# Performance work log

Hardware: AMD Instinct MI355X
Metric: run time of the kernel (lower is better)

The kernel has to match this reference:

```python
import jax, jax.numpy as jnp
import numpy as np
import math

N_RES, N_EDGE = 10000, 320000
C_S, C_Z, C_H, H, PQ, PV = 384, 128, 16, 12, 4, 8
INF, EPS = 1e5, 1e-8


def _lin(key, din, dout):
    k1, k2 = jax.random.split(key)
    w = jax.random.normal(k1, (din, dout), jnp.float32) * (1.0 / np.sqrt(din))
    b = jax.random.normal(k2, (dout,), jnp.float32) * 0.02
    return w, b


def setup_inputs() -> dict:
    key = jax.random.key(0)
    ks = jax.random.split(key, 16)
    s = jax.random.normal(ks[0], (N_RES, C_S), jnp.float32)
    z = jax.random.normal(ks[1], (N_EDGE, C_Z), jnp.float32)
    edge_index = jax.random.randint(ks[2], (2, N_EDGE), 0, N_RES, jnp.int32)
    rot = jnp.linalg.qr(jax.random.normal(ks[3], (N_RES, 3, 3), jnp.float32))[0]
    trans = jax.random.normal(ks[4], (N_RES, 3), jnp.float32)
    mask = jnp.ones((N_RES,), jnp.float32)
    wq, bq = _lin(ks[5], C_S, H * C_H)
    wkv, bkv = _lin(ks[6], C_S, 2 * H * C_H)
    wqp, bqp = _lin(ks[7], C_S, H * PQ * 3)
    wkvp, bkvp = _lin(ks[8], C_S, H * (PQ + PV) * 3)
    wb, bb = _lin(ks[9], C_Z, H)
    wdz, bdz = _lin(ks[10], C_Z, C_Z // 4)
    head_w = jax.random.normal(ks[11], (H,), jnp.float32) * 0.1
    wout, bout = _lin(ks[12], H * (C_Z // 4 + C_H + PV * 4), C_S)
    return dict(s=s, z=z, rot=rot, trans=trans, mask=mask, edge_index=edge_index,
                wq=wq, bq=bq, wkv=wkv, bkv=bkv, wqp=wqp, bqp=bqp, wkvp=wkvp, bkvp=bkvp,
                wb=wb, bb=bb, wdz=wdz, bdz=bdz, head_w=head_w, wout=wout, bout=bout)


def reference(s, z, rot, trans, mask, edge_index, wq, bq, wkv, bkv, wqp, bqp,
              wkvp, bkvp, wb, bb, wdz, bdz, head_w, wout, bout):
    n = s.shape[0]
    src, dst = edge_index[0], edge_index[1]  # key-side, query-side

    q = (s @ wq + bq).reshape(n, H, C_H)
    kv = (s @ wkv + bkv).reshape(n, H, 2 * C_H)
    k, v = kv[..., :C_H], kv[..., C_H:]

    def make_pts(x, p):
        # torch: split [n, H*p*3] into 3 chunks of H*p, stack on last dim -> [n, H*p, 3]
        x = jnp.stack(jnp.split(x, 3, axis=-1), axis=-1)
        x = jnp.einsum('nij,npj->npi', rot, x) + trans[:, None, :]  # global frame
        return x.reshape(n, H, p, 3)

    q_pts = make_pts(s @ wqp + bqp, PQ)                 # [n, H, PQ, 3]
    kv_pts = make_pts(s @ wkvp + bkvp, PQ + PV)
    k_pts, v_pts = kv_pts[..., :PQ, :], kv_pts[..., PQ:, :]

    b = z @ wb + bb                                      # [E, H]
    a = jnp.einsum('ehc,ehc->eh', q[dst], k[src]) * math.sqrt(1.0 / (3 * C_H))
    a = a + math.sqrt(1.0 / 3) * b

    disp = q_pts[dst] - k_pts[src]                       # [E, H, PQ, 3]
    hw = jax.nn.softplus(head_w) * math.sqrt(1.0 / (3 * (PQ * 9.0 / 2)))
    pt_att = -0.5 * jnp.einsum('ehp,h->eh', jnp.sum(disp * disp, axis=-1), hw)

    edge_mask = INF * (mask[src] * mask[dst] - 1.0)
    a = a + pt_att + edge_mask[:, None]

    # segment softmax over edges grouped by destination node
    m = jax.lax.stop_gradient(jax.ops.segment_max(a, dst, num_segments=n))
    ea = jnp.exp(a - m[dst])
    a = ea / (jax.ops.segment_sum(ea, dst, num_segments=n)[dst] + 1e-16)

    o = jax.ops.segment_sum(a[..., None] * v[src], dst, num_segments=n).reshape(n, -1)

    o_pt = jax.ops.segment_sum(a[..., None, None] * v_pts[src], dst, num_segments=n)  # [n,H,PV,3]
    o_pt = jnp.einsum('nji,nhpj->nhpi', rot, o_pt - trans[:, None, None, :])  # invert_apply
    o_pt_norm = jnp.sqrt(jnp.sum(o_pt * o_pt, axis=-1) + EPS).reshape(n, -1)
    o_pt = o_pt.reshape(n, H * PV, 3)

    pair_z = z @ wdz + bdz                               # [E, c_z//4]
    o_pair = jax.ops.segment_sum(a[..., None] * pair_z[:, None, :], dst,
                                 num_segments=n).reshape(n, -1)

    feats = jnp.concatenate([o, o_pt[..., 0], o_pt[..., 1], o_pt[..., 2],
                             o_pt_norm, o_pair], axis=-1)
    return feats @ wout + bout
```

## Files before the change

kernel.cpp:

```cpp
#include <hip/hip_runtime.h>
#include <hip/hip_bf16.h>
#include <math.h>

#define N_RESC 10000
#define N_EDGEC 320000
#define C_SC 384
#define C_ZC 128
#define AGG_D 864
#define FEAT_D 960
#define OUT_D 384

#define S1C 0.14433756729740643f
#define S2C 0.5773502691896258f
#define SHWC 0.13608276348795434f

__global__ void k_zero(int* cursor) {
    int i = blockIdx.x * 256 + threadIdx.x;
    if (i < N_RESC) cursor[i] = 0;
}

__global__ void k_hist(const int* __restrict__ ei, int* cursor) {
    int e = blockIdx.x * 256 + threadIdx.x;
    if (e < N_EDGEC) atomicAdd(&cursor[ei[N_EDGEC + e]], 1);
}

__global__ __launch_bounds__(1024) void k_scan(int* cursor, int* rowptr) {
    __shared__ int buf[1024];
    __shared__ int carry_s;
    int t = threadIdx.x;
    if (t == 0) carry_s = 0;
    __syncthreads();
    for (int ch = 0; ch < 10; ++ch) {
        int idx = ch * 1024 + t;
        int v = (idx < N_RESC) ? cursor[idx] : 0;
        buf[t] = v;
        __syncthreads();
        for (int off = 1; off < 1024; off <<= 1) {
            int x = (t >= off) ? buf[t - off] : 0;
            __syncthreads();
            buf[t] += x;
            __syncthreads();
        }
        int incl = buf[t];
        int excl = incl - v;
        int base = carry_s;
        int total = buf[1023];
        if (idx < N_RESC) { rowptr[idx] = base + excl; cursor[idx] = base + excl; }
        __syncthreads();
        if (t == 0) carry_s = base + total;
        __syncthreads();
    }
    if (t == 0) rowptr[N_RESC] = carry_s;
}

__global__ void k_scatter(const int* __restrict__ ei, int* cursor, int* csr,
                          int* src_csr, int* epos) {
    int e = blockIdx.x * 256 + threadIdx.x;
    if (e < N_EDGEC) {
        int d = ei[N_EDGEC + e];
        int s = ei[e];
        int pos = atomicAdd(&cursor[d], 1);
        csr[pos] = e;
        src_csr[pos] = s;
        epos[e] = pos;
    }
}

__global__ __launch_bounds__(256) void k_wpack(
    const float* __restrict__ wq, const float* __restrict__ bq,
    const float* __restrict__ wkv, const float* __restrict__ bkv,
    const float* __restrict__ wqp, const float* __restrict__ bqp,
    const float* __restrict__ wkvp, const float* __restrict__ bkvp,
    float* __restrict__ wpack, float* __restrict__ bpack) {
    int idx = blockIdx.x * 256 + threadIdx.x;
    if (idx < 384 * 1152) {
        int j = idx / 1152, c = idx % 1152;
        float v;
        if (c < 192)      v = wq[j * 192 + c];
        else if (c < 576) v = wkv[j * 384 + (c - 192)];
        else if (c < 720) v = wqp[j * 144 + (c - 576)];
        else              v = wkvp[j * 432 + (c - 720)];
        wpack[idx] = v;
    }
    if (idx < 1152) {
        float b;
        if (idx < 192)      b = bq[idx];
        else if (idx < 576) b = bkv[idx - 192];
        else if (idx < 720) b = bqp[idx - 576];
        else                b = bkvp[idx - 720];
        bpack[idx] = b;
    }
}

#define BM 64
#define BN 128
#define BK 32
__global__ __launch_bounds__(256) void k_proj(const float* __restrict__ s,
    const float* __restrict__ wpack, const float* __restrict__ bpack,
    float* __restrict__ qh, float* __restrict__ kh, float* __restrict__ vh,
    float* __restrict__ praw) {
    __shared__ float sT[BK][BM + 4];
    __shared__ float wt[BK][BN];
    int t = threadIdx.x;
    int bm0 = blockIdx.x * BM;
    int bn0 = blockIdx.y * BN;
    int tcol = t & 31;
    int trow = t >> 5;
    int c0 = tcol * 4;
    int r0 = trow * 8;

    int srow = t >> 2;
    int skoff = (t & 3) * 8;
    int gsrow = min(bm0 + srow, N_RESC - 1);
    const float* srcp = s + (long)gsrow * C_SC + skoff;

    float acc[8][4];
    #pragma unroll
    for (int i = 0; i < 8; i++)
        #pragma unroll
        for (int j = 0; j < 4; j++) acc[i][j] = 0.f;

    for (int k0 = 0; k0 < C_SC; k0 += BK) {
        float4 sa = *(const float4*)(srcp + k0);
        float4 sb = *(const float4*)(srcp + k0 + 4);
        sT[skoff + 0][srow] = sa.x; sT[skoff + 1][srow] = sa.y;
        sT[skoff + 2][srow] = sa.z; sT[skoff + 3][srow] = sa.w;
        sT[skoff + 4][srow] = sb.x; sT[skoff + 5][srow] = sb.y;
        sT[skoff + 6][srow] = sb.z; sT[skoff + 7][srow] = sb.w;
        #pragma unroll
        for (int q = 0; q < 4; q++) {
            int kk = (t >> 5) + q * 8;
            *(float4*)&wt[kk][c0] =
                *(const float4*)(wpack + (long)(k0 + kk) * 1152 + bn0 + c0);
        }
        __syncthreads();
        #pragma unroll
        for (int k = 0; k < BK; k++) {
            float4 a0 = *(const float4*)&sT[k][r0];
            float4 a1 = *(const float4*)&sT[k][r0 + 4];
            float4 b  = *(const float4*)&wt[k][c0];
            float av0 = a0.x, av1 = a0.y, av2 = a0.z, av3 = a0.w;
            float av4 = a1.x, av5 = a1.y, av6 = a1.z, av7 = a1.w;
            acc[0][0] = fmaf(av0, b.x, acc[0][0]); acc[0][1] = fmaf(av0, b.y, acc[0][1]);
            acc[0][2] = fmaf(av0, b.z, acc[0][2]); acc[0][3] = fmaf(av0, b.w, acc[0][3]);
            acc[1][0] = fmaf(av1, b.x, acc[1][0]); acc[1][1] = fmaf(av1, b.y, acc[1][1]);
            acc[1][2] = fmaf(av1, b.z, acc[1][2]); acc[1][3] = fmaf(av1, b.w, acc[1][3]);
            acc[2][0] = fmaf(av2, b.x, acc[2][0]); acc[2][1] = fmaf(av2, b.y, acc[2][1]);
            acc[2][2] = fmaf(av2, b.z, acc[2][2]); acc[2][3] = fmaf(av2, b.w, acc[2][3]);
            acc[3][0] = fmaf(av3, b.x, acc[3][0]); acc[3][1] = fmaf(av3, b.y, acc[3][1]);
            acc[3][2] = fmaf(av3, b.z, acc[3][2]); acc[3][3] = fmaf(av3, b.w, acc[3][3]);
            acc[4][0] = fmaf(av4, b.x, acc[4][0]); acc[4][1] = fmaf(av4, b.y, acc[4][1]);
            acc[4][2] = fmaf(av4, b.z, acc[4][2]); acc[4][3] = fmaf(av4, b.w, acc[4][3]);
            acc[5][0] = fmaf(av5, b.x, acc[5][0]); acc[5][1] = fmaf(av5, b.y, acc[5][1]);
            acc[5][2] = fmaf(av5, b.z, acc[5][2]); acc[5][3] = fmaf(av5, b.w, acc[5][3]);
            acc[6][0] = fmaf(av6, b.x, acc[6][0]); acc[6][1] = fmaf(av6, b.y, acc[6][1]);
            acc[6][2] = fmaf(av6, b.z, acc[6][2]); acc[6][3] = fmaf(av6, b.w, acc[6][3]);
            acc[7][0] = fmaf(av7, b.x, acc[7][0]); acc[7][1] = fmaf(av7, b.y, acc[7][1]);
            acc[7][2] = fmaf(av7, b.z, acc[7][2]); acc[7][3] = fmaf(av7, b.w, acc[7][3]);
        }
        __syncthreads();
    }
    #pragma unroll
    for (int j = 0; j < 4; j++) {
        int c = bn0 + c0 + j;
        float bv = bpack[c];
        #pragma unroll
        for (int i = 0; i < 8; i++) {
            int n = bm0 + r0 + i;
            if (n < N_RESC) {
                float val = acc[i][j] + bv;
                if (c < 192) qh[(long)n * 192 + c] = val;
                else if (c < 576) {
                    int cc = c - 192; int h = cc >> 5, r = cc & 31;
                    if (r < 16) kh[(long)n * 192 + h * 16 + r] = val;
                    else        vh[(long)n * 192 + h * 16 + (r - 16)] = val;
                } else praw[(long)n * 576 + (c - 576)] = val;
            }
        }
    }
}

__global__ __launch_bounds__(192) void k_rot(const float* __restrict__ praw,
    const float* __restrict__ rot, const float* __restrict__ trans,
    float* __restrict__ qpts, float* __restrict__ kpts, float* __restrict__ vpts) {
    int n = blockIdx.x;
    int t = threadIdx.x;
    __shared__ float R[9], T[3];
    if (t < 9) R[t] = rot[n * 9 + t];
    if (t < 3) T[t] = trans[n * 3 + t];
    __syncthreads();
    const float* pr = praw + (long)n * 576;
    if (t < 48) {
        float x0 = pr[t], x1 = pr[48 + t], x2 = pr[96 + t];
        #pragma unroll
        for (int i = 0; i < 3; i++)
            qpts[(long)n * 144 + t * 3 + i] = R[i*3+0]*x0 + R[i*3+1]*x1 + R[i*3+2]*x2 + T[i];
    } else {
        int p = t - 48;
        float x0 = pr[144 + p], x1 = pr[288 + p], x2 = pr[432 + p];
        int h = p / 12, pp = p % 12;
        #pragma unroll
        for (int i = 0; i < 3; i++) {
            float val = R[i*3+0]*x0 + R[i*3+1]*x1 + R[i*3+2]*x2 + T[i];
            if (pp < 4) kpts[(long)n * 144 + (h * 4 + pp) * 3 + i] = val;
            else        vpts[(long)n * 288 + (h * 8 + (pp - 4)) * 3 + i] = val;
        }
    }
}

__global__ __launch_bounds__(256) void k_zproj(const float* __restrict__ z,
    const int* __restrict__ epos,
    const float* __restrict__ wb, const float* __restrict__ bb,
    const float* __restrict__ wdz, const float* __restrict__ bdz,
    float* __restrict__ b_e, float* __restrict__ pairz) {
    __shared__ float zl[256][33];
    int t = threadIdx.x;
    long e0 = (long)blockIdx.x * 256;
    const float* zbase = z + e0 * C_ZC;
    float acc[44];
    #pragma unroll
    for (int c = 0; c < 12; c++) acc[c] = bb[c];
    #pragma unroll
    for (int c = 0; c < 32; c++) acc[12 + c] = bdz[c];

    for (int ch = 0; ch < 4; ch++) {
        __syncthreads();
        #pragma unroll
        for (int k = 0; k < 8; k++) {
            int idx4 = t + k * 256;
            int row = idx4 >> 3, j4 = idx4 & 7;
            float4 v = *(const float4*)(zbase + (long)row * C_ZC + ch * 32 + j4 * 4);
            zl[row][j4 * 4 + 0] = v.x;
            zl[row][j4 * 4 + 1] = v.y;
            zl[row][j4 * 4 + 2] = v.z;
            zl[row][j4 * 4 + 3] = v.w;
        }
        __syncthreads();
        #pragma unroll
        for (int j = 0; j < 32; j++) {
            float zs = zl[t][j];
            int jg = ch * 32 + j;
            #pragma unroll
            for (int c = 0; c < 12; c++) acc[c] = fmaf(zs, wb[jg * 12 + c], acc[c]);
            #pragma unroll
            for (int c = 0; c < 32; c++) acc[12 + c] = fmaf(zs, wdz[jg * 32 + c], acc[12 + c]);
        }
    }
    long pos = epos[e0 + t];
    float4* bo = reinterpret_cast<float4*>(b_e + pos * 12);
    #pragma unroll
    for (int q = 0; q < 3; q++)
        bo[q] = make_float4(acc[q*4], acc[q*4+1], acc[q*4+2], acc[q*4+3]);
    float4* po = reinterpret_cast<float4*>(pairz + pos * 32);
    #pragma unroll
    for (int q = 0; q < 8; q++)
        po[q] = make_float4(acc[12+q*4], acc[12+q*4+1], acc[12+q*4+2], acc[12+q*4+3]);
}

#define CAPL 256
__global__ __launch_bounds__(256) void k_logit(const int* __restrict__ rowptr,
    const int* __restrict__ src_csr,
    const float* __restrict__ qh, const float* __restrict__ kh,
    const float* __restrict__ qpts, const float* __restrict__ kpts,
    const float* __restrict__ mask, const float* __restrict__ head_w,
    const float* __restrict__ b_e, float* __restrict__ alog) {
    int n = blockIdx.x;
    int t = threadIdx.x;
    __shared__ float qf[192], qp[144], hws[12];
    __shared__ int slist[CAPL];
    if (t < 192) qf[t] = qh[(long)n * 192 + t];
    if (t < 144) qp[t] = qpts[(long)n * 144 + t];
    if (t < 12)  hws[t] = log1pf(expf(head_w[t])) * SHWC;
    float mdst = mask[n];
    int row0 = rowptr[n];
    int deg = rowptr[n + 1] - row0;
    int w = t >> 6, l = t & 63, c = l & 15, hq = l >> 4;
    for (int cs = 0; cs < deg; cs += CAPL) {
        int cnt = min(CAPL, deg - cs);
        __syncthreads();
        for (int i = t; i < cnt; i += 256) slist[i] = src_csr[row0 + cs + i];
        __syncthreads();
        for (int i = w * 2; i < cnt; i += 8) {
            int i1 = min(i + 1, cnt - 1);
            int s0 = slist[i], s1 = slist[i1];
            int pos0 = row0 + cs + i, pos1 = row0 + cs + i1;
            float em0 = 100000.0f * (mask[s0] * mdst - 1.0f);
            float em1 = 100000.0f * (mask[s1] * mdst - 1.0f);
            float kv0[3], kv1[3];
            #pragma unroll
            for (int tp = 0; tp < 3; tp++) {
                kv0[tp] = kh[(long)s0 * 192 + tp * 64 + l];
                kv1[tp] = kh[(long)s1 * 192 + tp * 64 + l];
            }
            float kp0[3] = {0.f,0.f,0.f}, kp1[3] = {0.f,0.f,0.f};
            if (c < 12) {
                #pragma unroll
                for (int tp = 0; tp < 3; tp++) {
                    int h = tp * 4 + hq;
                    kp0[tp] = kpts[(long)s0 * 144 + h * 12 + c];
                    kp1[tp] = kpts[(long)s1 * 144 + h * 12 + c];
                }
            }
            float be0[3] = {0.f,0.f,0.f}, be1[3] = {0.f,0.f,0.f};
            if (c == 0) {
                #pragma unroll
                for (int tp = 0; tp < 3; tp++) {
                    int h = tp * 4 + hq;
                    be0[tp] = b_e[(long)pos0 * 12 + h];
                    be1[tp] = b_e[(long)pos1 * 12 + h];
                }
            }
            #pragma unroll
            for (int tp = 0; tp < 3; tp++) {
                int h = tp * 4 + hq;
                float qfv = S1C * qf[h * 16 + c];
                float val0 = qfv * kv0[tp];
                float val1 = qfv * kv1[tp];
                if (c < 12) {
                    float qpv = qp[h * 12 + c];
                    float hw = -0.5f * hws[h];
                    float d0 = qpv - kp0[tp];
                    float d1 = qpv - kp1[tp];
                    val0 = fmaf(hw * d0, d0, val0);
                    val1 = fmaf(hw * d1, d1, val1);
                }
                val0 += __shfl_xor(val0, 8, 16); val1 += __shfl_xor(val1, 8, 16);
                val0 += __shfl_xor(val0, 4, 16); val1 += __shfl_xor(val1, 4, 16);
                val0 += __shfl_xor(val0, 2, 16); val1 += __shfl_xor(val1, 2, 16);
                val0 += __shfl_xor(val0, 1, 16); val1 += __shfl_xor(val1, 1, 16);
                if (c == 0) {
                    alog[(long)pos0 * 12 + h] = val0 + S2C * be0[tp] + em0;
                    if (i1 != i)
                        alog[(long)pos1 * 12 + h] = val1 + S2C * be1[tp] + em1;
                }
            }
        }
    }
}

#define CAPE 256
__global__ __launch_bounds__(256) void k_agg(const int* __restrict__ rowptr,
    const int* __restrict__ src_csr,
    const float* __restrict__ alog, const float* __restrict__ vh,
    const float* __restrict__ vpts, const float* __restrict__ pairz,
    float* __restrict__ agg) {
    int n = blockIdx.x;
    int t = threadIdx.x;
    __shared__ float red[16 * 12];
    __shared__ float mh[12], linv[12];
    __shared__ float al[CAPE * 12];
    __shared__ int sl_[CAPE];
    int row0 = rowptr[n];
    int deg = rowptr[n + 1] - row0;
    int g = t >> 4, l16 = t & 15;
    if (l16 < 12) {
        float lm = -1e30f;
        for (int i = g; i < deg; i += 16)
            lm = fmaxf(lm, alog[(long)(row0 + i) * 12 + l16]);
        red[g * 12 + l16] = lm;
    }
    __syncthreads();
    if (t < 12) {
        float m = -1e30f;
        for (int gg = 0; gg < 16; gg++) m = fmaxf(m, red[gg * 12 + t]);
        mh[t] = m;
    }
    __syncthreads();
    if (l16 < 12) {
        float m = mh[l16];
        float ls = 0.f;
        for (int i = g; i < deg; i += 16)
            ls += expf(alog[(long)(row0 + i) * 12 + l16] - m);
        red[g * 12 + l16] = ls;
    }
    __syncthreads();
    if (t < 12) {
        float ssum = 0.f;
        for (int gg = 0; gg < 16; gg++) ssum += red[gg * 12 + t];
        linv[t] = 1.f / (ssum + 1e-16f);
    }

    const float* base = nullptr;
    int scale = 0, hk = 0, use_e = 0;
    int comp = t * 4;
    if (comp < 192)      { base = vh + comp; scale = 192; hk = comp >> 4; }
    else if (comp < 480) { int idx = comp - 192; base = vpts + idx; scale = 288; hk = idx / 24; }
    else if (comp < 864) { int idx = comp - 480; base = pairz + (idx & 31); scale = 32; hk = idx >> 5; use_e = 1; }
    float4 acc = make_float4(0.f, 0.f, 0.f, 0.f);

    for (int cs = 0; cs < deg; cs += CAPE) {
        int cnt = min(CAPE, deg - cs);
        int p0 = row0 + cs;
        __syncthreads();
        for (int i = t; i < cnt * 12; i += 256) {
            int h = i % 12;
            al[i] = expf(alog[(long)p0 * 12 + i] - mh[h]) * linv[h];
        }
        for (int i = t; i < cnt; i += 256) sl_[i] = src_csr[p0 + i];
        __syncthreads();
        if (t < 216) {
            int i = 0;
            for (; i + 4 <= cnt; i += 4) {
                int i0 = use_e ? (p0 + i)     : sl_[i];
                int i1 = use_e ? (p0 + i + 1) : sl_[i+1];
                int i2 = use_e ? (p0 + i + 2) : sl_[i+2];
                int i3 = use_e ? (p0 + i + 3) : sl_[i+3];
                float4 v0 = *(const float4*)(base + (long)i0 * scale);
                float4 v1 = *(const float4*)(base + (long)i1 * scale);
                float4 v2 = *(const float4*)(base + (long)i2 * scale);
                float4 v3 = *(const float4*)(base + (long)i3 * scale);
                float w0 = al[i * 12 + hk];
                float w1 = al[(i+1) * 12 + hk];
                float w2 = al[(i+2) * 12 + hk];
                float w3 = al[(i+3) * 12 + hk];
                acc.x = fmaf(w0, v0.x, acc.x); acc.y = fmaf(w0, v0.y, acc.y);
                acc.z = fmaf(w0, v0.z, acc.z); acc.w = fmaf(w0, v0.w, acc.w);
                acc.x = fmaf(w1, v1.x, acc.x); acc.y = fmaf(w1, v1.y, acc.y);
                acc.z = fmaf(w1, v1.z, acc.z); acc.w = fmaf(w1, v1.w, acc.w);
                acc.x = fmaf(w2, v2.x, acc.x); acc.y = fmaf(w2, v2.y, acc.y);
                acc.z = fmaf(w2, v2.z, acc.z); acc.w = fmaf(w2, v2.w, acc.w);
                acc.x = fmaf(w3, v3.x, acc.x); acc.y = fmaf(w3, v3.y, acc.y);
                acc.z = fmaf(w3, v3.z, acc.z); acc.w = fmaf(w3, v3.w, acc.w);
            }
            for (; i < cnt; i++) {
                int ii = use_e ? (p0 + i) : sl_[i];
                float4 v = *(const float4*)(base + (long)ii * scale);
                float w = al[i * 12 + hk];
                acc.x = fmaf(w, v.x, acc.x); acc.y = fmaf(w, v.y, acc.y);
                acc.z = fmaf(w, v.z, acc.z); acc.w = fmaf(w, v.w, acc.w);
            }
        }
    }
    if (t < 216) *(float4*)(agg + (long)n * AGG_D + comp) = acc;
}

#define NT_F 8
__global__ __launch_bounds__(192) void k_final(const float* __restrict__ agg,
    const float* __restrict__ rot, const float* __restrict__ trans,
    const float* __restrict__ wout, const float* __restrict__ bout,
    float* __restrict__ out) {
    __shared__ float f[NT_F][FEAT_D];
    int t = threadIdx.x;
    int node0 = blockIdx.x * NT_F;
    for (int idx = t; idx < NT_F * 192; idx += 192) {
        int nt = idx / 192, c = idx % 192;
        f[nt][c] = agg[(long)(node0 + nt) * AGG_D + c];
    }
    for (int idx = t; idx < NT_F * 96; idx += 192) {
        int nt = idx / 96, p = idx % 96;
        int n = node0 + nt;
        const float* a = agg + (long)n * AGG_D;
        float gx = a[192 + p * 3 + 0] - trans[n * 3 + 0];
        float gy = a[192 + p * 3 + 1] - trans[n * 3 + 1];
        float gz = a[192 + p * 3 + 2] - trans[n * 3 + 2];
        const float* R = rot + (long)n * 9;
        float lx = R[0] * gx + R[3] * gy + R[6] * gz;
        float ly = R[1] * gx + R[4] * gy + R[7] * gz;
        float lz = R[2] * gx + R[5] * gy + R[8] * gz;
        f[nt][192 + p] = lx;
        f[nt][288 + p] = ly;
        f[nt][384 + p] = lz;
        f[nt][480 + p] = sqrtf(lx * lx + ly * ly + lz * lz + 1e-8f);
    }
    for (int idx = t; idx < NT_F * 384; idx += 192) {
        int nt = idx / 384, q = idx % 384;
        f[nt][576 + q] = agg[(long)(node0 + nt) * AGG_D + 480 + q];
    }
    __syncthreads();
    float acc0[NT_F], acc1[NT_F];
    float b0 = bout[t], b1 = bout[t + 192];
    #pragma unroll
    for (int nt = 0; nt < NT_F; nt++) { acc0[nt] = b0; acc1[nt] = b1; }
    for (int j = 0; j < FEAT_D; j += 4) {
        float4 fv[NT_F];
        #pragma unroll
        for (int nt = 0; nt < NT_F; nt++) fv[nt] = *(const float4*)&f[nt][j];
        #pragma unroll
        for (int u = 0; u < 4; u++) {
            float w0 = wout[(j + u) * OUT_D + t];
            float w1 = wout[(j + u) * OUT_D + t + 192];
            #pragma unroll
            for (int nt = 0; nt < NT_F; nt++) {
                float fvu = (u == 0) ? fv[nt].x : (u == 1) ? fv[nt].y : (u == 2) ? fv[nt].z : fv[nt].w;
                acc0[nt] = fmaf(fvu, w0, acc0[nt]);
                acc1[nt] = fmaf(fvu, w1, acc1[nt]);
            }
        }
    }
    #pragma unroll
    for (int nt = 0; nt < NT_F; nt++) {
        out[(long)(node0 + nt) * OUT_D + t] = acc0[nt];
        out[(long)(node0 + nt) * OUT_D + t + 192] = acc1[nt];
    }
}

extern "C" void kernel_launch(void* const* d_in, const int* in_sizes, int n_in,
                              void* d_out, int out_size, void* d_ws, size_t ws_size,
                              hipStream_t stream) {
    const float* s     = (const float*)d_in[0];
    const float* z     = (const float*)d_in[1];
    const float* rot   = (const float*)d_in[2];
    const float* trans = (const float*)d_in[3];
    const float* mask  = (const float*)d_in[4];
    const int*   ei    = (const int*)d_in[5];
    const float* wq    = (const float*)d_in[6];
    const float* bq    = (const float*)d_in[7];
    const float* wkv   = (const float*)d_in[8];
    const float* bkv   = (const float*)d_in[9];
    const float* wqp   = (const float*)d_in[10];
    const float* bqp   = (const float*)d_in[11];
    const float* wkvp  = (const float*)d_in[12];
    const float* bkvp  = (const float*)d_in[13];
    const float* wb    = (const float*)d_in[14];
    const float* bb    = (const float*)d_in[15];
    const float* wdz   = (const float*)d_in[16];
    const float* bdz   = (const float*)d_in[17];
    const float* head_w= (const float*)d_in[18];
    const float* wout  = (const float*)d_in[19];
    const float* bout  = (const float*)d_in[20];
    float* out = (float*)d_out;

    float* ws    = (float*)d_ws;
    float* qh    = ws;
    float* kh    = qh + 1920000;
    float* vh    = kh + 1920000;
    float* qpts  = vh + 1920000;
    float* kpts  = qpts + 1440000;
    float* vpts  = kpts + 1440000;
    float* b_e   = vpts + 2880000;
    float* pairz = b_e + 3840000;
    float* alog  = pairz + 10240000;
    float* agg   = alog + 3840000;
    float* praw  = agg;
    float* wpack = agg + 5760000;
    float* bpack = wpack + 442368;
    int* rowptr  = (int*)(agg + 8640000);
    int* cursor  = rowptr + 10004;
    int* csr     = cursor + 10000;
    int* src_csr = csr + N_EDGEC;
    int* epos    = src_csr + N_EDGEC;

    k_zero<<<(N_RESC + 255) / 256, 256, 0, stream>>>(cursor);
    k_hist<<<(N_EDGEC + 255) / 256, 256, 0, stream>>>(ei, cursor);
    k_scan<<<1, 1024, 0, stream>>>(cursor, rowptr);
    k_scatter<<<(N_EDGEC + 255) / 256, 256, 0, stream>>>(ei, cursor, csr, src_csr, epos);

    k_wpack<<<(384 * 1152 + 255) / 256, 256, 0, stream>>>(wq, bq, wkv, bkv, wqp, bqp,
                                                          wkvp, bkvp, wpack, bpack);
    dim3 pgrid((N_RESC + BM - 1) / BM, 1152 / BN);
    k_proj<<<pgrid, 256, 0, stream>>>(s, wpack, bpack, qh, kh, vh, praw);
    k_rot<<<N_RESC, 192, 0, stream>>>(praw, rot, trans, qpts, kpts, vpts);

    k_zproj<<<N_EDGEC / 256, 256, 0, stream>>>(z, epos, wb, bb, wdz, bdz, b_e, pairz);

    k_logit<<<N_RESC, 256, 0, stream>>>(rowptr, src_csr, qh, kh, qpts, kpts,
                                        mask, head_w, b_e, alog);

    k_agg<<<N_RESC, 256, 0, stream>>>(rowptr, src_csr, alog, vh, vpts, pairz, agg);

    k_final<<<N_RESC / NT_F, 192, 0, stream>>>(agg, rot, trans, wout, bout, out);
}
```

Before: 916.3 us.

## Retile z projection as register-blocked GEMM with packed LDS weights

The z-projection kernel is restructured from one edge per thread with 44 accumulators that read weights straight from global memory. It becomes a register-blocked tile: each thread computes 4 edges by 6 output columns, z is held transposed in LDS, and a packed, padded 128x48 weight matrix sits in shared memory. The weight pack kernel now also builds this combined wb/wdz matrix and bias. The aim is to cut global weight-load traffic and register pressure so the FMAs run from LDS with reuse. In exchange, output stores become scattered float2 writes across threads, and some compute is spent on 4 padding columns.

```diff
diff --git a/kernel.cpp b/kernel.cpp
--- a/kernel.cpp
+++ b/kernel.cpp
@@ -71,7 +71,10 @@
     const float* __restrict__ wkv, const float* __restrict__ bkv,
     const float* __restrict__ wqp, const float* __restrict__ bqp,
     const float* __restrict__ wkvp, const float* __restrict__ bkvp,
-    float* __restrict__ wpack, float* __restrict__ bpack) {
+    const float* __restrict__ wb, const float* __restrict__ bb,
+    const float* __restrict__ wdz, const float* __restrict__ bdz,
+    float* __restrict__ wpack, float* __restrict__ bpack,
+    float* __restrict__ wzpack, float* __restrict__ bzpack) {
     int idx = blockIdx.x * 256 + threadIdx.x;
     if (idx < 384 * 1152) {
         int j = idx / 1152, c = idx % 1152;
@@ -89,6 +92,19 @@
         else if (idx < 720) b = bqp[idx - 576];
         else                b = bkvp[idx - 720];
         bpack[idx] = b;
+    }
+    if (idx < 128 * 48) {
+        int j = idx / 48, c = idx % 48;
+        float v = 0.f;
+        if (c < 12)      v = wb[j * 12 + c];
+        else if (c < 44) v = wdz[j * 32 + (c - 12)];
+        wzpack[idx] = v;
+    }
+    if (idx < 48) {
+        float b = 0.f;
+        if (idx < 12)      b = bb[idx];
+        else if (idx < 44) b = bdz[idx - 12];
+        bzpack[idx] = b;
     }
 }
 
@@ -208,53 +224,88 @@
     }
 }
 
+#define ZBM 128
 __global__ __launch_bounds__(256) void k_zproj(const float* __restrict__ z,
     const int* __restrict__ epos,
-    const float* __restrict__ wb, const float* __restrict__ bb,
-    const float* __restrict__ wdz, const float* __restrict__ bdz,
+    const float* __restrict__ wzpack, const float* __restrict__ bzpack,
     float* __restrict__ b_e, float* __restrict__ pairz) {
-    __shared__ float zl[256][33];
+    __shared__ float zT[32][ZBM + 4];
+    __shared__ float wl[128][48];
     int t = threadIdx.x;
-    long e0 = (long)blockIdx.x * 256;
-    const float* zbase = z + e0 * C_ZC;
-    float acc[44];
+    long e0 = (long)blockIdx.x * ZBM;
+    int er = t & 31;
+    int cg = t >> 5;
+    int cb = cg * 6;
+
     #pragma unroll
-    for (int c = 0; c < 12; c++) acc[c] = bb[c];
+    for (int q = 0; q < 6; q++) {
+        int f = t + q * 256;
+        int row = f / 12, c4 = f % 12;
+        *(float4*)&wl[row][c4 * 4] = *(const float4*)(wzpack + row * 48 + c4 * 4);
+    }
+
+    float acc[4][6];
     #pragma unroll
-    for (int c = 0; c < 32; c++) acc[12 + c] = bdz[c];
-
-    for (int ch = 0; ch < 4; ch++) {
-        __syncthreads();
-        #pragma unroll
-        for (int k = 0; k < 8; k++) {
-            int idx4 = t + k * 256;
-            int row = idx4 >> 3, j4 = idx4 & 7;
-            float4 v = *(const float4*)(zbase + (long)row * C_ZC + ch * 32 + j4 * 4);
-            zl[row][j4 * 4 + 0] = v.x;
-            zl[row][j4 * 4 + 1] = v.y;
-            zl[row][j4 * 4 + 2] = v.z;
-            zl[row][j4 * 4 + 3] = v.w;
-        }
-        __syncthreads();
-        #pragma unroll
-        for (int j = 0; j < 32; j++) {
-            float zs = zl[t][j];
-            int jg = ch * 32 + j;
-            #pragma unroll
-            for (int c = 0; c < 12; c++) acc[c] = fmaf(zs, wb[jg * 12 + c], acc[c]);
-            #pragma unroll
-            for (int c = 0; c < 32; c++) acc[12 + c] = fmaf(zs, wdz[jg * 32 + c], acc[12 + c]);
-        }
-    }
-    long pos = epos[e0 + t];
-    float4* bo = reinterpret_cast<float4*>(b_e + pos * 12);
+    for (int i = 0; i < 4; i++)
+        #pragma unroll
+        for (int j = 0; j < 6; j++) acc[i][j] = 0.f;
+
+    int r = t >> 1, ch2 = t & 1;
+    const float* zp = z + (e0 + r) * C_ZC + ch2 * 16;
+
+    for (int kc = 0; kc < 4; kc++) {
+        __syncthreads();
+        #pragma unroll
+        for (int q = 0; q < 4; q++) {
+            float4 v = *(const float4*)(zp + kc * 32 + q * 4);
+            int kk = ch2 * 16 + q * 4;
+            zT[kk + 0][r] = v.x; zT[kk + 1][r] = v.y;
+            zT[kk + 2][r] = v.z; zT[kk + 3][r] = v.w;
+        }
+        __syncthreads();
+        #pragma unroll
+        for (int k = 0; k < 32; k++) {
+            float4 zv = *(const float4*)&zT[k][er * 4];
+            const float* wrow = &wl[kc * 32 + k][cb];
+            float w0 = wrow[0], w1 = wrow[1], w2 = wrow[2];
+            float w3 = wrow[3], w4 = wrow[4], w5 = wrow[5];
+            acc[0][0] = fmaf(zv.x, w0, acc[0][0]); acc[0][1] = fmaf(zv.x, w1, acc[0][1]);
+            acc[0][2] = fmaf(zv.x, w2, acc[0][2]); acc[0][3] = fmaf(zv.x, w3, acc[0][3]);
+            acc[0][4] = fmaf(zv.x, w4, acc[0][4]); acc[0][5] = fmaf(zv.x, w5, acc[0][5]);
+            acc[1][0] = fmaf(zv.y, w0, acc[1][0]); acc[1][1] = fmaf(zv.y, w1, acc[1][1]);
+            acc[1][2] = fmaf(zv.y, w2, acc[1][2]); acc[1][3] = fmaf(zv.y, w3, acc[1][3]);
+            acc[1][4] = fmaf(zv.y, w4, acc[1][4]); acc[1][5] = fmaf(zv.y, w5, acc[1][5]);
+            acc[2][0] = fmaf(zv.z, w0, acc[2][0]); acc[2][1] = fmaf(zv.z, w1, acc[2][1]);
+            acc[2][2] = fmaf(zv.z, w2, acc[2][2]); acc[2][3] = fmaf(zv.z, w3, acc[2][3]);
+            acc[2][4] = fmaf(zv.z, w4, acc[2][4]); acc[2][5] = fmaf(zv.z, w5, acc[2][5]);
+            acc[3][0] = fmaf(zv.w, w0, acc[3][0]); acc[3][1] = fmaf(zv.w, w1, acc[3][1]);
+            acc[3][2] = fmaf(zv.w, w2, acc[3][2]); acc[3][3] = fmaf(zv.w, w3, acc[3][3]);
+            acc[3][4] = fmaf(zv.w, w4, acc[3][4]); acc[3][5] = fmaf(zv.w, w5, acc[3][5]);
+        }
+    }
+
+    float bz0 = bzpack[cb + 0], bz1 = bzpack[cb + 1], bz2 = bzpack[cb + 2];
+    float bz3 = bzpack[cb + 3], bz4 = bzpack[cb + 4], bz5 = bzpack[cb + 5];
     #pragma unroll
-    for (int q = 0; q < 3; q++)
-        bo[q] = make_float4(acc[q*4], acc[q*4+1], acc[q*4+2], acc[q*4+3]);
-    float4* po = reinterpret_cast<float4*>(pairz + pos * 32);
-    #pragma unroll
-    for (int q = 0; q < 8; q++)
-        po[q] = make_float4(acc[12+q*4], acc[12+q*4+1], acc[12+q*4+2], acc[12+q*4+3]);
+    for (int ei = 0; ei < 4; ei++) {
+        long pos = epos[e0 + er * 4 + ei];
+        float o0 = acc[ei][0] + bz0, o1 = acc[ei][1] + bz1;
+        float o2 = acc[ei][2] + bz2, o3 = acc[ei][3] + bz3;
+        float o4 = acc[ei][4] + bz4, o5 = acc[ei][5] + bz5;
+        if (cb < 12) {
+            float* d = b_e + pos * 12 + cb;
+            *(float2*)(d + 0) = make_float2(o0, o1);
+            *(float2*)(d + 2) = make_float2(o2, o3);
+            *(float2*)(d + 4) = make_float2(o4, o5);
+        } else if (cb < 42) {
+            float* d = pairz + pos * 32 + (cb - 12);
+            *(float2*)(d + 0) = make_float2(o0, o1);
+            *(float2*)(d + 2) = make_float2(o2, o3);
+            *(float2*)(d + 4) = make_float2(o4, o5);
+        } else {
+            *(float2*)(pairz + pos * 32 + 30) = make_float2(o0, o1);
+        }
+    }
 }
 
 #define CAPL 256
@@ -534,6 +585,8 @@
     float* praw  = agg;
     float* wpack = agg + 5760000;
     float* bpack = wpack + 442368;
+    float* wzpack= bpack + 1152;
+    float* bzpack= wzpack + 6144;
     int* rowptr  = (int*)(agg + 8640000);
     int* cursor  = rowptr + 10004;
     int* csr     = cursor + 10000;
@@ -546,12 +599,13 @@
     k_scatter<<<(N_EDGEC + 255) / 256, 256, 0, stream>>>(ei, cursor, csr, src_csr, epos);
 
     k_wpack<<<(384 * 1152 + 255) / 256, 256, 0, stream>>>(wq, bq, wkv, bkv, wqp, bqp,
-                                                          wkvp, bkvp, wpack, bpack);
+                                                          wkvp, bkvp, wb, bb, wdz, bdz,
+                                                          wpack, bpack, wzpack, bzpack);
     dim3 pgrid((N_RESC + BM - 1) / BM, 1152 / BN);
     k_proj<<<pgrid, 256, 0, stream>>>(s, wpack, bpack, qh, kh, vh, praw);
     k_rot<<<N_RESC, 192, 0, stream>>>(praw, rot, trans, qpts, kpts, vpts);
 
-    k_zproj<<<N_EDGEC / 256, 256, 0, stream>>>(z, epos, wb, bb, wdz, bdz, b_e, pairz);
+    k_zproj<<<N_EDGEC / ZBM, 256, 0, stream>>>(z, epos, wzpack, bzpack, b_e, pairz);
 
     k_logit<<<N_RESC, 256, 0, stream>>>(rowptr, src_csr, qh, kh, qpts, kpts,
                                         mask, head_w, b_e, alog);
```

After: 800.8 us. 1.14x faster.
